# Optimization experiments

Hardware: AMD Instinct MI355X
Metric: run time of the kernel (lower is better)

The kernel has to match this reference:

```python
import jax, jax.numpy as jnp
import numpy as np

WIDTHS = [16384, 4096, 1024, 16]
LATENT = WIDTHS[-1]

# static polynomial-library index sets (poly_order = 3)
_PAIRS = np.array([(i, j) for i in range(LATENT) for j in range(i, LATENT)]).T
_TRIPS = np.array([(i, j, k) for i in range(LATENT) for j in range(i, LATENT) for k in range(j, LATENT)]).T


def sindy_library(z):
    # [1]*d ++ z ++ upper-tri pairwise products ++ upper-tri triple products -> [984]
    ones = jnp.ones((LATENT,), dtype=z.dtype)
    quad = z[_PAIRS[0]] * z[_PAIRS[1]]
    cub = z[_TRIPS[0]] * z[_TRIPS[1]] * z[_TRIPS[2]]
    return jnp.concatenate([ones, z, quad, cub])


def setup_inputs() -> dict:
    key = jax.random.key(0)
    ks = jax.random.split(key, 32)
    d = {
        'x': jax.random.normal(ks[0], (WIDTHS[0],), dtype=jnp.float32),
        'dx': jax.random.normal(ks[1], (WIDTHS[0],), dtype=jnp.float32),
        'ddx': jax.random.normal(ks[2], (WIDTHS[0],), dtype=jnp.float32),
    }
    ki = 3
    # encoder Linear(widths[i], widths[i+1]); xavier-ish scale
    for i in range(len(WIDTHS) - 1):
        fin, fout = WIDTHS[i], WIDTHS[i + 1]
        s = jnp.sqrt(2.0 / (fin + fout)).astype(jnp.float32)
        d[f'we_w{i}'] = jax.random.normal(ks[ki], (fout, fin), dtype=jnp.float32) * s; ki += 1
        d[f'we_b{i}'] = jax.random.normal(ks[ki], (fout,), dtype=jnp.float32) * 0.01; ki += 1
    # decoder Linear(widths[-i-1], widths[-i-2])
    for i in range(len(WIDTHS) - 1):
        fin, fout = WIDTHS[-i - 1], WIDTHS[-i - 2]
        s = jnp.sqrt(2.0 / (fin + fout)).astype(jnp.float32)
        d[f'wd_w{i}'] = jax.random.normal(ks[ki], (fout, fin), dtype=jnp.float32) * s; ki += 1
        d[f'wd_b{i}'] = jax.random.normal(ks[ki], (fout,), dtype=jnp.float32) * 0.01; ki += 1
    sindy_dim = 2 * LATENT + _PAIRS.shape[1] + _TRIPS.shape[1]  # 984
    d['E_w'] = jnp.ones((LATENT, sindy_dim), dtype=jnp.float32)  # nn.init.ones_
    d['E_b'] = jnp.zeros((LATENT,), dtype=jnp.float32)
    return d


def reference(x, dx, ddx,
              we_w0, we_b0, we_w1, we_b1, we_w2, we_b2,
              wd_w0, wd_b0, wd_w1, wd_b1, wd_w2, wd_b2,
              E_w, E_b):
    def enc(v):
        h = jax.nn.sigmoid(we_w0 @ v + we_b0)
        h = jax.nn.sigmoid(we_w1 @ h + we_b1)
        return we_w2 @ h + we_b2  # identity on last layer

    def dec(v):
        h = jax.nn.sigmoid(wd_w0 @ v + wd_b0)
        h = jax.nn.sigmoid(wd_w1 @ h + wd_b1)
        return wd_w2 @ h + wd_b2

    z = enc(x)                                   # [latent]
    gx_enc = jax.jacrev(enc)(x)                  # [latent, input_dim]
    dz = gx_enc @ dx                             # [latent]
    theta = sindy_library(z)                     # [sindy_dim]
    dzb = E_w @ theta + E_b                      # [latent]
    xb = dec(z)                                  # [input_dim]
    gx_dec = jax.jacfwd(dec)(z)                  # [input_dim, latent]
    dxb = gx_dec @ dzb                           # [input_dim]
    return (z, dz, dzb, xb, dxb)
```

## Files before the change

kernel.cpp:

```cpp
#include <hip/hip_runtime.h>
#include <math.h>

typedef float vfloat4 __attribute__((ext_vector_type(4)));

template <int NCOLS, bool SIG>
__global__ __launch_bounds__(256) void gemv_dual(
    const float* __restrict__ W, const float* __restrict__ b,
    const float* __restrict__ v, const float* __restrict__ t,
    float* __restrict__ h_out, float* __restrict__ t_out, int nrows)
{
    constexpr int NV = NCOLS / 4;
    constexpr int ITER = NV / 64;
    const int lane = threadIdx.x & 63;
    const int wave = (int)((blockIdx.x * blockDim.x + threadIdx.x) >> 6);
    const int nw = (int)((gridDim.x * blockDim.x) >> 6);
    const vfloat4* __restrict__ v4 = (const vfloat4*)v;
    const vfloat4* __restrict__ t4 = (const vfloat4*)t;

    for (int row = wave; row < nrows; row += nw) {
        const vfloat4* __restrict__ W4 = (const vfloat4*)(W + (size_t)row * NCOLS);
        float ah = 0.f, at = 0.f;
        #pragma unroll 4
        for (int k = 0; k < ITER; ++k) {
            const int i = lane + 64 * k;
            vfloat4 w = __builtin_nontemporal_load(&W4[i]);
            vfloat4 a = v4[i];
            vfloat4 c = t4[i];
            ah += w.x * a.x + w.y * a.y + w.z * a.z + w.w * a.w;
            at += w.x * c.x + w.y * c.y + w.z * c.z + w.w * c.w;
        }
        #pragma unroll
        for (int off = 32; off; off >>= 1) {
            ah += __shfl_down(ah, off, 64);
            at += __shfl_down(at, off, 64);
        }
        if (lane == 0) {
            ah += b[row];
            if (SIG) {
                float s = 1.f / (1.f + expf(-ah));
                h_out[row] = s;
                t_out[row] = s * (1.f - s) * at;
            } else {
                h_out[row] = ah;
                t_out[row] = at;
            }
        }
    }
}

__global__ __launch_bounds__(1024) void head_kernel(
    const float* __restrict__ W2, const float* __restrict__ b2,
    const float* __restrict__ h2, const float* __restrict__ t2,
    const float* __restrict__ Ew, const float* __restrict__ Eb,
    const float* __restrict__ U0, const float* __restrict__ c0,
    float* __restrict__ out,
    float* __restrict__ g1, float* __restrict__ s1)
{
    __shared__ float z_s[16], dz_s[16], dzb_s[16];
    __shared__ float theta[984];

    const int tid = threadIdx.x;
    const int lane = tid & 63;
    const int r = tid >> 6;

    {
        const vfloat4* Wr = (const vfloat4*)(W2 + r * 1024);
        const vfloat4* h4 = (const vfloat4*)h2;
        const vfloat4* t4 = (const vfloat4*)t2;
        float ah = 0.f, at = 0.f;
        #pragma unroll
        for (int k = 0; k < 4; ++k) {
            const int i = lane + 64 * k;
            vfloat4 w = Wr[i];
            vfloat4 a = h4[i];
            vfloat4 c = t4[i];
            ah += w.x * a.x + w.y * a.y + w.z * a.z + w.w * a.w;
            at += w.x * c.x + w.y * c.y + w.z * c.z + w.w * c.w;
        }
        #pragma unroll
        for (int off = 32; off; off >>= 1) {
            ah += __shfl_down(ah, off, 64);
            at += __shfl_down(at, off, 64);
        }
        if (lane == 0) {
            z_s[r] = ah + b2[r];
            dz_s[r] = at;
        }
    }
    __syncthreads();

    if (tid < 16) { theta[tid] = 1.0f; theta[16 + tid] = z_s[tid]; }
    for (int t = tid; t < 136; t += 1024) {
        int rem = t, i = 0;
        while (rem >= 16 - i) { rem -= 16 - i; i++; }
        theta[32 + t] = z_s[i] * z_s[i + rem];
    }
    for (int t = tid; t < 816; t += 1024) {
        int rem = t, i = 0;
        for (;;) { int cnt = (16 - i) * (17 - i) >> 1; if (rem < cnt) break; rem -= cnt; i++; }
        int j = i;
        while (rem >= 16 - j) { rem -= 16 - j; j++; }
        theta[168 + t] = z_s[i] * z_s[j] * z_s[j + rem];
    }
    __syncthreads();

    {
        const vfloat4* Er = (const vfloat4*)(Ew + r * 984);
        const vfloat4* th4 = (const vfloat4*)theta;
        float a = 0.f;
        for (int i = lane; i < 246; i += 64) {
            vfloat4 w = Er[i];
            vfloat4 x = th4[i];
            a += w.x * x.x + w.y * x.y + w.z * x.z + w.w * x.w;
        }
        #pragma unroll
        for (int off = 32; off; off >>= 1) a += __shfl_down(a, off, 64);
        if (lane == 0) dzb_s[r] = a + Eb[r];
    }
    __syncthreads();

    if (tid < 16) {
        out[tid]      = z_s[tid];
        out[16 + tid] = dz_s[tid];
        out[32 + tid] = dzb_s[tid];
    }

    {
        const vfloat4* U4 = (const vfloat4*)(U0 + tid * 16);
        float ah = 0.f, at = 0.f;
        #pragma unroll
        for (int q = 0; q < 4; ++q) {
            vfloat4 w = U4[q];
            ah += w.x * z_s[4*q] + w.y * z_s[4*q+1] + w.z * z_s[4*q+2] + w.w * z_s[4*q+3];
            at += w.x * dzb_s[4*q] + w.y * dzb_s[4*q+1] + w.z * dzb_s[4*q+2] + w.w * dzb_s[4*q+3];
        }
        ah += c0[tid];
        float s = 1.f / (1.f + expf(-ah));
        g1[tid] = s;
        s1[tid] = s * (1.f - s) * at;
    }
}

extern "C" void kernel_launch(void* const* d_in, const int* in_sizes, int n_in,
                              void* d_out, int out_size, void* d_ws, size_t ws_size,
                              hipStream_t stream)
{
    const float* x     = (const float*)d_in[0];
    const float* dx    = (const float*)d_in[1];
    const float* we_w0 = (const float*)d_in[3];
    const float* we_b0 = (const float*)d_in[4];
    const float* we_w1 = (const float*)d_in[5];
    const float* we_b1 = (const float*)d_in[6];
    const float* we_w2 = (const float*)d_in[7];
    const float* we_b2 = (const float*)d_in[8];
    const float* wd_w0 = (const float*)d_in[9];
    const float* wd_b0 = (const float*)d_in[10];
    const float* wd_w1 = (const float*)d_in[11];
    const float* wd_b1 = (const float*)d_in[12];
    const float* wd_w2 = (const float*)d_in[13];
    const float* wd_b2 = (const float*)d_in[14];
    const float* E_w   = (const float*)d_in[15];
    const float* E_b   = (const float*)d_in[16];

    float* out = (float*)d_out;
    float* ws  = (float*)d_ws;

    float* h1 = ws;
    float* t1 = ws + 4096;
    float* h2 = ws + 8192;
    float* t2 = ws + 9216;
    float* g1 = ws + 10240;
    float* s1 = ws + 11264;
    float* g2 = ws + 12288;
    float* s2 = ws + 16384;

    float* xb  = out + 48;
    float* dxb = out + 48 + 16384;

    gemv_dual<16384, true><<<1024, 256, 0, stream>>>(we_w0, we_b0, x, dx, h1, t1, 4096);
    gemv_dual<4096, true><<<256, 256, 0, stream>>>(we_w1, we_b1, h1, t1, h2, t2, 1024);
    head_kernel<<<1, 1024, 0, stream>>>(we_w2, we_b2, h2, t2, E_w, E_b,
                                        wd_w0, wd_b0, out, g1, s1);
    gemv_dual<1024, true><<<1024, 256, 0, stream>>>(wd_w1, wd_b1, g1, s1, g2, s2, 4096);
    gemv_dual<4096, false><<<4096, 256, 0, stream>>>(wd_w2, wd_b2, g2, s2, xb, dxb, 16384);
}
```

Measured before the change: 552.2 us.

## Fuse all encoder/decoder stages into one persistent kernel with grid barriers

Replaces five separate kernel launches with one persistent 1024-block kernel. The stages are separated by atomic-counter grid barriers, and the counter is reset with a memset before each launch. The first layer becomes a split-K GEMV: each block computes 16 rows over a quarter of the columns and keeps its x/dx slice in registers, then partial sums are reduced after a barrier. The goal is to remove launch gaps and tail inefficiency between the dependent GEMVs. It also relies on all 1024 blocks being co-resident, has a timeout guard on the spin wait, and leaves the grid idle during the single-block head stage.

```diff
diff --git a/kernel.cpp b/kernel.cpp
--- a/kernel.cpp
+++ b/kernel.cpp
@@ -3,141 +3,270 @@
 
 typedef float vfloat4 __attribute__((ext_vector_type(4)));
 
-template <int NCOLS, bool SIG>
-__global__ __launch_bounds__(256) void gemv_dual(
-    const float* __restrict__ W, const float* __restrict__ b,
-    const float* __restrict__ v, const float* __restrict__ t,
-    float* __restrict__ h_out, float* __restrict__ t_out, int nrows)
+#define NBLK 1024u
+
+__device__ __forceinline__ float dot4(vfloat4 a, vfloat4 b) {
+    return a.x * b.x + a.y * b.y + a.z * b.z + a.w * b.w;
+}
+
+__device__ __forceinline__ void reduce2(float& a, float& b) {
+#pragma unroll
+    for (int off = 32; off; off >>= 1) {
+        a += __shfl_down(a, off, 64);
+        b += __shfl_down(b, off, 64);
+    }
+}
+
+__device__ __forceinline__ void gridbar(unsigned* cnt, unsigned target) {
+    __syncthreads();
+    if (threadIdx.x == 0) {
+        __threadfence();
+        __hip_atomic_fetch_add(cnt, 1u, __ATOMIC_RELEASE, __HIP_MEMORY_SCOPE_AGENT);
+        unsigned guard = 0;
+        while (__hip_atomic_load(cnt, __ATOMIC_ACQUIRE, __HIP_MEMORY_SCOPE_AGENT) < target) {
+            __builtin_amdgcn_s_sleep(2);
+            if (++guard > 30000000u) break;
+        }
+        __threadfence();
+    }
+    __syncthreads();
+}
+
+__global__ __launch_bounds__(256, 4) void sindy_fused(
+    const float* __restrict__ x, const float* __restrict__ dx,
+    const float* __restrict__ we_w0, const float* __restrict__ we_b0,
+    const float* __restrict__ we_w1, const float* __restrict__ we_b1,
+    const float* __restrict__ we_w2, const float* __restrict__ we_b2,
+    const float* __restrict__ wd_w0, const float* __restrict__ wd_b0,
+    const float* __restrict__ wd_w1, const float* __restrict__ wd_b1,
+    const float* __restrict__ wd_w2, const float* __restrict__ wd_b2,
+    const float* __restrict__ Ew, const float* __restrict__ Eb,
+    float* __restrict__ h1, float* __restrict__ t1,
+    float* __restrict__ h2, float* __restrict__ t2,
+    float* __restrict__ g1, float* __restrict__ s1,
+    float* __restrict__ g2, float* __restrict__ s2,
+    float* __restrict__ part1, unsigned* __restrict__ bar,
+    float* __restrict__ out, float* __restrict__ xb, float* __restrict__ dxb)
 {
-    constexpr int NV = NCOLS / 4;
-    constexpr int ITER = NV / 64;
-    const int lane = threadIdx.x & 63;
-    const int wave = (int)((blockIdx.x * blockDim.x + threadIdx.x) >> 6);
-    const int nw = (int)((gridDim.x * blockDim.x) >> 6);
-    const vfloat4* __restrict__ v4 = (const vfloat4*)v;
-    const vfloat4* __restrict__ t4 = (const vfloat4*)t;
-
-    for (int row = wave; row < nrows; row += nw) {
-        const vfloat4* __restrict__ W4 = (const vfloat4*)(W + (size_t)row * NCOLS);
+    __shared__ float red[4][16][2];
+    __shared__ __align__(16) float theta[984];
+    __shared__ float z_s[16], dz_s[16], dzb_s[16];
+
+    const int tid  = (int)threadIdx.x;
+    const int lane = tid & 63;
+    const int w    = tid >> 6;
+    const int b    = (int)blockIdx.x;
+
+    {
+        const int g  = b >> 2;
+        const int jb = b & 3;
+        const int c  = (jb << 2) + w;
+        const int r0 = g << 4;
+        const vfloat4* x4 = (const vfloat4*)x;
+        const vfloat4* d4 = (const vfloat4*)dx;
+        vfloat4 vv[4], tt[4];
+#pragma unroll
+        for (int k = 0; k < 4; ++k) {
+            const int i = c * 256 + k * 64 + lane;
+            vv[k] = x4[i];
+            tt[k] = d4[i];
+        }
+        const vfloat4* W4 = (const vfloat4*)we_w0;
+#pragma unroll 2
+        for (int r = 0; r < 16; ++r) {
+            const vfloat4* Wr = W4 + (size_t)(r0 + r) * 4096 + (size_t)c * 256;
+            float ah = 0.f, at = 0.f;
+#pragma unroll
+            for (int k = 0; k < 4; ++k) {
+                vfloat4 wv = __builtin_nontemporal_load(&Wr[k * 64 + lane]);
+                ah += dot4(wv, vv[k]);
+                at += dot4(wv, tt[k]);
+            }
+            reduce2(ah, at);
+            if (lane == 0) { red[w][r][0] = ah; red[w][r][1] = at; }
+        }
+        __syncthreads();
+        if (tid < 32) {
+            const int r = tid >> 1, s = tid & 1;
+            float sum = red[0][r][s] + red[1][r][s] + red[2][r][s] + red[3][r][s];
+            part1[((size_t)(r0 + r) * 2 + s) * 4 + jb] = sum;
+        }
+    }
+    gridbar(bar, 1u * NBLK);
+
+    {
+        const int gt = b * 256 + tid;
+        if (gt < 4096) {
+            const vfloat4* p4 = (const vfloat4*)part1;
+            vfloat4 ph = p4[gt * 2];
+            vfloat4 pt = p4[gt * 2 + 1];
+            float ah = ph.x + ph.y + ph.z + ph.w + we_b0[gt];
+            float at = pt.x + pt.y + pt.z + pt.w;
+            float sg = 1.f / (1.f + expf(-ah));
+            h1[gt] = sg;
+            t1[gt] = sg * (1.f - sg) * at;
+        }
+    }
+    gridbar(bar, 2u * NBLK);
+
+    {
+        const vfloat4* W4 = (const vfloat4*)we_w1 + (size_t)b * 1024;
+        const vfloat4* v4 = (const vfloat4*)h1;
+        const vfloat4* t4 = (const vfloat4*)t1;
         float ah = 0.f, at = 0.f;
-        #pragma unroll 4
-        for (int k = 0; k < ITER; ++k) {
-            const int i = lane + 64 * k;
-            vfloat4 w = __builtin_nontemporal_load(&W4[i]);
-            vfloat4 a = v4[i];
-            vfloat4 c = t4[i];
-            ah += w.x * a.x + w.y * a.y + w.z * a.z + w.w * a.w;
-            at += w.x * c.x + w.y * c.y + w.z * c.z + w.w * c.w;
-        }
-        #pragma unroll
-        for (int off = 32; off; off >>= 1) {
-            ah += __shfl_down(ah, off, 64);
-            at += __shfl_down(at, off, 64);
-        }
-        if (lane == 0) {
-            ah += b[row];
-            if (SIG) {
-                float s = 1.f / (1.f + expf(-ah));
-                h_out[row] = s;
-                t_out[row] = s * (1.f - s) * at;
-            } else {
-                h_out[row] = ah;
-                t_out[row] = at;
-            }
-        }
-    }
-}
-
-__global__ __launch_bounds__(1024) void head_kernel(
-    const float* __restrict__ W2, const float* __restrict__ b2,
-    const float* __restrict__ h2, const float* __restrict__ t2,
-    const float* __restrict__ Ew, const float* __restrict__ Eb,
-    const float* __restrict__ U0, const float* __restrict__ c0,
-    float* __restrict__ out,
-    float* __restrict__ g1, float* __restrict__ s1)
-{
-    __shared__ float z_s[16], dz_s[16], dzb_s[16];
-    __shared__ float theta[984];
-
-    const int tid = threadIdx.x;
-    const int lane = tid & 63;
-    const int r = tid >> 6;
-
-    {
-        const vfloat4* Wr = (const vfloat4*)(W2 + r * 1024);
+#pragma unroll
+        for (int k = 0; k < 4; ++k) {
+            const int i = w * 256 + k * 64 + lane;
+            vfloat4 wv = __builtin_nontemporal_load(&W4[i]);
+            ah += dot4(wv, v4[i]);
+            at += dot4(wv, t4[i]);
+        }
+        reduce2(ah, at);
+        if (lane == 0) { red[w][0][0] = ah; red[w][0][1] = at; }
+        __syncthreads();
+        if (tid == 0) {
+            float A = red[0][0][0] + red[1][0][0] + red[2][0][0] + red[3][0][0] + we_b1[b];
+            float T = red[0][0][1] + red[1][0][1] + red[2][0][1] + red[3][0][1];
+            float sg = 1.f / (1.f + expf(-A));
+            h2[b] = sg;
+            t2[b] = sg * (1.f - sg) * T;
+        }
+    }
+    gridbar(bar, 3u * NBLK);
+
+    if (b == 0) {
         const vfloat4* h4 = (const vfloat4*)h2;
         const vfloat4* t4 = (const vfloat4*)t2;
+#pragma unroll
+        for (int rr = 0; rr < 4; ++rr) {
+            const int row = (rr << 2) + w;
+            const vfloat4* Wr = (const vfloat4*)we_w2 + (size_t)row * 256;
+            float ah = 0.f, at = 0.f;
+#pragma unroll
+            for (int k = 0; k < 4; ++k) {
+                const int i = k * 64 + lane;
+                vfloat4 wv = Wr[i];
+                ah += dot4(wv, h4[i]);
+                at += dot4(wv, t4[i]);
+            }
+            reduce2(ah, at);
+            if (lane == 0) { z_s[row] = ah + we_b2[row]; dz_s[row] = at; }
+        }
+        __syncthreads();
+
+        if (tid < 16) { theta[tid] = 1.0f; theta[16 + tid] = z_s[tid]; }
+        for (int t5 = tid; t5 < 136; t5 += 256) {
+            int rem = t5, i = 0;
+            while (rem >= 16 - i) { rem -= 16 - i; i++; }
+            theta[32 + t5] = z_s[i] * z_s[i + rem];
+        }
+        for (int t5 = tid; t5 < 816; t5 += 256) {
+            int rem = t5, i = 0;
+            for (;;) { int cnt = (16 - i) * (17 - i) >> 1; if (rem < cnt) break; rem -= cnt; i++; }
+            int j = i;
+            while (rem >= 16 - j) { rem -= 16 - j; j++; }
+            theta[168 + t5] = z_s[i] * z_s[j] * z_s[j + rem];
+        }
+        __syncthreads();
+
+        const vfloat4* th4 = (const vfloat4*)theta;
+#pragma unroll
+        for (int rr = 0; rr < 4; ++rr) {
+            const int row = (rr << 2) + w;
+            const vfloat4* Er = (const vfloat4*)Ew + (size_t)row * 246;
+            float a = 0.f;
+#pragma unroll
+            for (int k = 0; k < 4; ++k) {
+                const int i = k * 64 + lane;
+                if (i < 246) a += dot4(Er[i], th4[i]);
+            }
+#pragma unroll
+            for (int off = 32; off; off >>= 1) a += __shfl_down(a, off, 64);
+            if (lane == 0) dzb_s[row] = a + Eb[row];
+        }
+        __syncthreads();
+
+        if (tid < 16) {
+            out[tid]      = z_s[tid];
+            out[16 + tid] = dz_s[tid];
+            out[32 + tid] = dzb_s[tid];
+        }
+
+#pragma unroll
+        for (int q = 0; q < 4; ++q) {
+            const int row = tid + (q << 8);
+            const vfloat4* U4 = (const vfloat4*)wd_w0 + (size_t)row * 4;
+            float ah = 0.f, at = 0.f;
+#pragma unroll
+            for (int p = 0; p < 4; ++p) {
+                vfloat4 u = U4[p];
+                ah += u.x * z_s[4*p] + u.y * z_s[4*p+1] + u.z * z_s[4*p+2] + u.w * z_s[4*p+3];
+                at += u.x * dzb_s[4*p] + u.y * dzb_s[4*p+1] + u.z * dzb_s[4*p+2] + u.w * dzb_s[4*p+3];
+            }
+            ah += wd_b0[row];
+            float sg = 1.f / (1.f + expf(-ah));
+            g1[row] = sg;
+            s1[row] = sg * (1.f - sg) * at;
+        }
+    }
+    gridbar(bar, 4u * NBLK);
+
+    {
+        const int row = (b << 2) + w;
+        const vfloat4* Wr = (const vfloat4*)wd_w1 + (size_t)row * 256;
+        const vfloat4* v4 = (const vfloat4*)g1;
+        const vfloat4* t4 = (const vfloat4*)s1;
         float ah = 0.f, at = 0.f;
-        #pragma unroll
+#pragma unroll
         for (int k = 0; k < 4; ++k) {
-            const int i = lane + 64 * k;
-            vfloat4 w = Wr[i];
-            vfloat4 a = h4[i];
-            vfloat4 c = t4[i];
-            ah += w.x * a.x + w.y * a.y + w.z * a.z + w.w * a.w;
-            at += w.x * c.x + w.y * c.y + w.z * c.z + w.w * c.w;
-        }
-        #pragma unroll
-        for (int off = 32; off; off >>= 1) {
-            ah += __shfl_down(ah, off, 64);
-            at += __shfl_down(at, off, 64);
-        }
+            const int i = k * 64 + lane;
+            vfloat4 wv = __builtin_nontemporal_load(&Wr[i]);
+            ah += dot4(wv, v4[i]);
+            at += dot4(wv, t4[i]);
+        }
+        reduce2(ah, at);
         if (lane == 0) {
-            z_s[r] = ah + b2[r];
-            dz_s[r] = at;
-        }
-    }
-    __syncthreads();
-
-    if (tid < 16) { theta[tid] = 1.0f; theta[16 + tid] = z_s[tid]; }
-    for (int t = tid; t < 136; t += 1024) {
-        int rem = t, i = 0;
-        while (rem >= 16 - i) { rem -= 16 - i; i++; }
-        theta[32 + t] = z_s[i] * z_s[i + rem];
-    }
-    for (int t = tid; t < 816; t += 1024) {
-        int rem = t, i = 0;
-        for (;;) { int cnt = (16 - i) * (17 - i) >> 1; if (rem < cnt) break; rem -= cnt; i++; }
-        int j = i;
-        while (rem >= 16 - j) { rem -= 16 - j; j++; }
-        theta[168 + t] = z_s[i] * z_s[j] * z_s[j + rem];
-    }
-    __syncthreads();
-
-    {
-        const vfloat4* Er = (const vfloat4*)(Ew + r * 984);
-        const vfloat4* th4 = (const vfloat4*)theta;
-        float a = 0.f;
-        for (int i = lane; i < 246; i += 64) {
-            vfloat4 w = Er[i];
-            vfloat4 x = th4[i];
-            a += w.x * x.x + w.y * x.y + w.z * x.z + w.w * x.w;
-        }
-        #pragma unroll
-        for (int off = 32; off; off >>= 1) a += __shfl_down(a, off, 64);
-        if (lane == 0) dzb_s[r] = a + Eb[r];
-    }
-    __syncthreads();
-
-    if (tid < 16) {
-        out[tid]      = z_s[tid];
-        out[16 + tid] = dz_s[tid];
-        out[32 + tid] = dzb_s[tid];
-    }
-
-    {
-        const vfloat4* U4 = (const vfloat4*)(U0 + tid * 16);
-        float ah = 0.f, at = 0.f;
-        #pragma unroll
-        for (int q = 0; q < 4; ++q) {
-            vfloat4 w = U4[q];
-            ah += w.x * z_s[4*q] + w.y * z_s[4*q+1] + w.z * z_s[4*q+2] + w.w * z_s[4*q+3];
-            at += w.x * dzb_s[4*q] + w.y * dzb_s[4*q+1] + w.z * dzb_s[4*q+2] + w.w * dzb_s[4*q+3];
-        }
-        ah += c0[tid];
-        float s = 1.f / (1.f + expf(-ah));
-        g1[tid] = s;
-        s1[tid] = s * (1.f - s) * at;
+            ah += wd_b1[row];
+            float sg = 1.f / (1.f + expf(-ah));
+            g2[row] = sg;
+            s2[row] = sg * (1.f - sg) * at;
+        }
+    }
+    gridbar(bar, 5u * NBLK);
+
+    {
+        const vfloat4* g4 = (const vfloat4*)g2;
+        const vfloat4* s4 = (const vfloat4*)s2;
+        vfloat4 vv[4], tt[4];
+#pragma unroll
+        for (int k = 0; k < 4; ++k) {
+            const int i = w * 256 + k * 64 + lane;
+            vv[k] = g4[i];
+            tt[k] = s4[i];
+        }
+        const int r0 = b << 4;
+        const vfloat4* W4 = (const vfloat4*)wd_w2;
+#pragma unroll 2
+        for (int r = 0; r < 16; ++r) {
+            const vfloat4* Wr = W4 + (size_t)(r0 + r) * 1024 + (size_t)w * 256;
+            float ah = 0.f, at = 0.f;
+#pragma unroll
+            for (int k = 0; k < 4; ++k) {
+                vfloat4 wv = __builtin_nontemporal_load(&Wr[k * 64 + lane]);
+                ah += dot4(wv, vv[k]);
+                at += dot4(wv, tt[k]);
+            }
+            reduce2(ah, at);
+            if (lane == 0) { red[w][r][0] = ah; red[w][r][1] = at; }
+        }
+        __syncthreads();
+        if (tid < 32) {
+            const int r = tid >> 1, s5 = tid & 1;
+            float tot = red[0][r][s5] + red[1][r][s5] + red[2][r][s5] + red[3][r][s5];
+            const int row = r0 + r;
+            if (s5 == 0) xb[row]  = tot + wd_b2[row];
+            else         dxb[row] = tot;
+        }
     }
 }
 
@@ -165,22 +294,24 @@
     float* out = (float*)d_out;
     float* ws  = (float*)d_ws;
 
-    float* h1 = ws;
-    float* t1 = ws + 4096;
-    float* h2 = ws + 8192;
-    float* t2 = ws + 9216;
-    float* g1 = ws + 10240;
-    float* s1 = ws + 11264;
-    float* g2 = ws + 12288;
-    float* s2 = ws + 16384;
+    float* h1    = ws;
+    float* t1    = ws + 4096;
+    float* h2    = ws + 8192;
+    float* t2    = ws + 9216;
+    float* g1    = ws + 10240;
+    float* s1    = ws + 11264;
+    float* g2    = ws + 12288;
+    float* s2    = ws + 16384;
+    float* part1 = ws + 20480;
+    unsigned* bar = (unsigned*)(ws + 53248);
 
     float* xb  = out + 48;
     float* dxb = out + 48 + 16384;
 
-    gemv_dual<16384, true><<<1024, 256, 0, stream>>>(we_w0, we_b0, x, dx, h1, t1, 4096);
-    gemv_dual<4096, true><<<256, 256, 0, stream>>>(we_w1, we_b1, h1, t1, h2, t2, 1024);
-    head_kernel<<<1, 1024, 0, stream>>>(we_w2, we_b2, h2, t2, E_w, E_b,
-                                        wd_w0, wd_b0, out, g1, s1);
-    gemv_dual<1024, true><<<1024, 256, 0, stream>>>(wd_w1, wd_b1, g1, s1, g2, s2, 4096);
-    gemv_dual<4096, false><<<4096, 256, 0, stream>>>(wd_w2, wd_b2, g2, s2, xb, dxb, 16384);
-}
+    hipMemsetAsync(bar, 0, 64, stream);
+
+    sindy_fused<<<dim3(NBLK), dim3(256), 0, stream>>>(
+        x, dx, we_w0, we_b0, we_w1, we_b1, we_w2, we_b2,
+        wd_w0, wd_b0, wd_w1, wd_b1, wd_w2, wd_b2, E_w, E_b,
+        h1, t1, h2, t2, g1, s1, g2, s2, part1, bar, out, xb, dxb);
+}
```

After: 1.357 ms. 146% more time.
